# Optimization experiments

Measured on AMD Instinct MI355X. Metric: run time of the kernel, lower is better.

## Reference

```python
import jax, jax.numpy as jnp
import numpy as np

NUM_USERS = 50000
NUM_ITEMS = 50000
N_NODES = NUM_USERS + NUM_ITEMS
NNZ = 3200000
EMB_DIM = 64
N_LAYERS = 3
BATCH = 16384


def setup_inputs() -> dict:
    key = jax.random.key(0)
    ks = jax.random.split(key, 7)
    user_emb = 0.1 * jax.random.normal(ks[0], (NUM_USERS, EMB_DIM), dtype=jnp.float32)
    item_emb = 0.1 * jax.random.normal(ks[1], (NUM_ITEMS, EMB_DIM), dtype=jnp.float32)
    edge_val = jax.random.uniform(ks[2], (NNZ,), dtype=jnp.float32)
    edge_src = jax.random.randint(ks[3], (NNZ,), 0, N_NODES, dtype=jnp.int32)
    edge_dst = jax.random.randint(ks[4], (NNZ,), 0, N_NODES, dtype=jnp.int32)
    users = jax.random.randint(ks[5], (BATCH,), 0, NUM_USERS, dtype=jnp.int32)
    items = jax.random.randint(ks[6], (BATCH,), 0, NUM_ITEMS, dtype=jnp.int32)
    return {"user_emb": user_emb, "item_emb": item_emb, "edge_val": edge_val,
            "edge_src": edge_src, "edge_dst": edge_dst, "users": users, "items": items}


def _computer(user_emb, item_emb, edge_val, edge_src, edge_dst):
    # LightGCN propagation: all_emb <- A @ all_emb, mean over layer outputs (incl. layer 0)
    all_emb = jnp.concatenate([user_emb, item_emb], axis=0)  # [N, D]
    acc = all_emb
    for _ in range(N_LAYERS):
        msg = edge_val[:, None] * all_emb[edge_src]          # [nnz, D]
        all_emb = jax.ops.segment_sum(msg, edge_dst, num_segments=N_NODES)
        acc = acc + all_emb
    light_out = acc / jnp.float32(N_LAYERS + 1)
    return light_out[:NUM_USERS], light_out[NUM_USERS:]


def reference(user_emb, item_emb, edge_val, edge_src, edge_dst, users, items):
    all_users, all_items = _computer(user_emb, item_emb, edge_val, edge_src, edge_dst)
    users_emb = all_users[users]                              # [B, D]
    items_emb = all_items[items]                              # [B, D]
    gamma = jnp.sum(users_emb * items_emb, axis=1)            # [B]
    return gamma
```

## Files before the change

kernel.cpp:

```cpp
#include <hip/hip_runtime.h>

#define NUM_USERS 50000
#define NUM_ITEMS 50000
#define N_NODES   100000
#define NNZ       3200000
#define EMB_DIM   64
#define N_LAYERS  3
#define BATCH     16384

#define NBUCK 512
#define ABITS 8
#define NODES_PER_BUCK 256
#define TILE_EDGES 8192
#define NBUCK_USED ((N_NODES + NODES_PER_BUCK - 1) / NODES_PER_BUCK)
#define CAP 9216

typedef unsigned long long ull;
typedef float v2f __attribute__((ext_vector_type(2)));

__device__ inline unsigned bf16pair(float a, float b) {
    unsigned ua = __float_as_uint(a), ub = __float_as_uint(b);
    unsigned r0 = (ua + 0x7fffu + ((ua >> 16) & 1u)) >> 16;
    unsigned r1 = (ub + 0x7fffu + ((ub >> 16) & 1u)) >> 16;
    return r0 | (r1 << 16);
}
__device__ inline float blo(unsigned u) { return __uint_as_float(u << 16); }
__device__ inline float bhi(unsigned u) { return __uint_as_float(u & 0xffff0000u); }

__device__ inline void pkfma(v2f& d, v2f a, v2f b) {
    asm("v_pk_fma_f32 %0, %1, %2, %0" : "+v"(d) : "v"(a), "v"(b));
}

__device__ inline void accP(v2f& sA, v2f& sB, v2f& sC, v2f& sD, uint4 g, unsigned r) {
    float w = (float)(r >> 17);
    v2f w2 = {w, w};
    v2f e0 = {blo(g.x), bhi(g.x)};
    v2f e1 = {blo(g.y), bhi(g.y)};
    v2f e2 = {blo(g.z), bhi(g.z)};
    v2f e3 = {blo(g.w), bhi(g.w)};
    pkfma(sA, e0, w2);
    pkfma(sB, e1, w2);
    pkfma(sC, e2, w2);
    pkfma(sD, e3, w2);
}

__device__ inline uint4 gath(const unsigned char* __restrict__ base, unsigned r, unsigned dOff) {
    unsigned off = ((r & 0x1FFFFu) << 7) + dOff;
    return *(const uint4*)(base + off);
}

__global__ void init_emb_kernel(const float* __restrict__ ue,
                                const float* __restrict__ ie,
                                unsigned* __restrict__ E0,
                                int* __restrict__ bucketCursor,
                                unsigned char* __restrict__ flags,
                                const int* __restrict__ users,
                                const int* __restrict__ items) {
    int idx = blockIdx.x * blockDim.x + threadIdx.x;
    if (blockIdx.x == 0 && threadIdx.x < 256) {
        bucketCursor[threadIdx.x]       = threadIdx.x * CAP;
        bucketCursor[threadIdx.x + 256] = (threadIdx.x + 256) * CAP;
    }
    if (idx < BATCH) {
        flags[users[idx]] = 1;
    } else if (idx < 2 * BATCH) {
        flags[NUM_USERS + items[idx - BATCH]] = 1;
    }
    const int total = N_NODES * (EMB_DIM / 4);
    if (idx >= total) return;
    const int uoff = NUM_USERS * (EMB_DIM / 4);
    float4 v;
    if (idx < uoff) v = ((const float4*)ue)[idx];
    else            v = ((const float4*)ie)[idx - uoff];
    uint2 h;
    h.x = bf16pair(v.x, v.y);
    h.y = bf16pair(v.z, v.w);
    ((uint2*)E0)[idx] = h;
}

__global__ void partA_kernel(const float* __restrict__ ev,
                             const int*  __restrict__ es,
                             const int*  __restrict__ ed,
                             int* __restrict__ bucketCursor,
                             ull* __restrict__ tmp) {
    __shared__ int hist[NBUCK];
    __shared__ int base[NBUCK];
    __shared__ int cnt2[NBUCK];
    int tid = threadIdx.x;
    int e0 = blockIdx.x * TILE_EDGES;

    int      mySrc[8], myDst[8];
    unsigned myQ[8];

    for (int i = tid; i < NBUCK; i += 1024) hist[i] = 0;
    __syncthreads();

    #pragma unroll
    for (int k = 0; k < 8; ++k) {
        int e = e0 + k * 1024 + tid;
        if (e < NNZ) {
            mySrc[k] = es[e];
            myDst[k] = ed[e];
            myQ[k]   = (unsigned)fminf(ev[e] * 32768.f + 0.5f, 32767.f);
            atomicAdd(&hist[((unsigned)myDst[k]) >> ABITS], 1);
        } else {
            myDst[k] = -1;
        }
    }
    __syncthreads();

    for (int i = tid; i < NBUCK; i += 1024) {
        int c = hist[i];
        base[i] = c ? atomicAdd(&bucketCursor[i], c) : 0;
        cnt2[i] = 0;
    }
    __syncthreads();

    #pragma unroll
    for (int k = 0; k < 8; ++k) {
        int dst = myDst[k];
        if (dst < 0) continue;
        int b = ((unsigned)dst) >> ABITS;
        int pos = base[b] + atomicAdd(&cnt2[b], 1);
        if (pos < (b + 1) * CAP) {
            ull rec = (ull)(unsigned)(mySrc[k] | ((dst & (NODES_PER_BUCK - 1)) << 17))
                    | ((ull)myQ[k] << 25);
            tmp[pos] = rec;
        }
    }
}

__global__ void partB_kernel(const ull* __restrict__ tmp,
                             const int* __restrict__ bucketCursor,
                             int* __restrict__ rowStart,
                             int* __restrict__ deg,
                             unsigned* __restrict__ sorted) {
    __shared__ int cnt[NODES_PER_BUCK];
    __shared__ int sc[NODES_PER_BUCK];
    __shared__ int cur[NODES_PER_BUCK];
    int b = blockIdx.x;
    int tid = threadIdx.x;
    int nodeLo = b << ABITS;
    int startE = b * CAP;
    int endE   = bucketCursor[b];

    if (tid < NODES_PER_BUCK) cnt[tid] = 0;
    __syncthreads();

    ull myRec[9];
    int nRec = 0;
    #pragma unroll
    for (int k = 0; k < 9; ++k) {
        int i = startE + k * 1024 + tid;
        if (i < endE) {
            myRec[k] = tmp[i];
            nRec = k + 1;
            atomicAdd(&cnt[(int)((myRec[k] >> 17) & (NODES_PER_BUCK - 1))], 1);
        }
    }
    __syncthreads();

    if (tid < NODES_PER_BUCK) sc[tid] = (cnt[tid] + 3) & ~3;
    __syncthreads();
    for (int o = 1; o < NODES_PER_BUCK; o <<= 1) {
        int add = 0;
        if (tid < NODES_PER_BUCK && tid >= o) add = sc[tid - o];
        __syncthreads();
        if (tid < NODES_PER_BUCK) sc[tid] += add;
        __syncthreads();
    }
    if (tid < NODES_PER_BUCK) {
        int node = nodeLo + tid;
        int pc = (cnt[tid] + 3) & ~3;
        int rs = startE + sc[tid] - pc;
        cur[tid] = rs;
        if (node < N_NODES) {
            rowStart[node] = rs;
            deg[node] = cnt[tid];
        }
    }
    __syncthreads();

    for (int k = 0; k < nRec; ++k) {
        ull rec = myRec[k];
        int dl = (int)((rec >> 17) & (NODES_PER_BUCK - 1));
        unsigned o = (unsigned)(rec & 0x1FFFFULL) | ((unsigned)((rec >> 25) & 0x7FFF) << 17);
        int pos = atomicAdd(&cur[dl], 1);
        if (pos < startE + CAP) sorted[pos] = o;
    }
}

__global__ void pull_kernel(const unsigned char* __restrict__ A16,
                            uint4* __restrict__ B16,
                            const unsigned* __restrict__ sorted,
                            const int* __restrict__ rowStart,
                            const int* __restrict__ deg,
                            const unsigned char* __restrict__ flags,
                            int gate) {
    int node = __builtin_amdgcn_readfirstlane((blockIdx.x << 2) + (threadIdx.x >> 6));
    if (node >= N_NODES) return;
    if (gate && flags[node] != 1) return;
    int lane = threadIdx.x & 63;
    int eg = lane >> 3;
    unsigned dOff = (unsigned)(lane & 7) << 4;
    int start = rowStart[node];
    int cnt   = deg[node];
    const unsigned* ep = sorted + start;

    v2f sA = {0.f, 0.f}, sB = {0.f, 0.f}, sC = {0.f, 0.f}, sD = {0.f, 0.f};
    int j = 0;
    while (j + 32 <= cnt) {
        uint4 R = *(const uint4*)(ep + j + (eg << 2));
        uint4 g0 = gath(A16, R.x, dOff);
        uint4 g1 = gath(A16, R.y, dOff);
        uint4 g2 = gath(A16, R.z, dOff);
        uint4 g3 = gath(A16, R.w, dOff);
        accP(sA, sB, sC, sD, g0, R.x);
        accP(sA, sB, sC, sD, g1, R.y);
        accP(sA, sB, sC, sD, g2, R.z);
        accP(sA, sB, sC, sD, g3, R.w);
        j += 32;
    }
    int rem = cnt - j;
    if (rem >= 16) {
        uint2 R = *(const uint2*)(ep + j + (eg << 1));
        uint4 g0 = gath(A16, R.x, dOff);
        uint4 g1 = gath(A16, R.y, dOff);
        accP(sA, sB, sC, sD, g0, R.x);
        accP(sA, sB, sC, sD, g1, R.y);
        j += 16; rem -= 16;
    }
    if (rem > 0) {
        int i0 = j + eg, i1 = j + 8 + eg;
        unsigned r0 = (i0 < cnt) ? ep[i0] : 0u;
        unsigned r1 = (i1 < cnt) ? ep[i1] : 0u;
        uint4 g0 = gath(A16, r0, dOff);
        uint4 g1 = gath(A16, r1, dOff);
        accP(sA, sB, sC, sD, g0, r0);
        accP(sA, sB, sC, sD, g1, r1);
    }

    sA.x += __shfl_xor(sA.x, 8, 64);  sA.y += __shfl_xor(sA.y, 8, 64);
    sB.x += __shfl_xor(sB.x, 8, 64);  sB.y += __shfl_xor(sB.y, 8, 64);
    sC.x += __shfl_xor(sC.x, 8, 64);  sC.y += __shfl_xor(sC.y, 8, 64);
    sD.x += __shfl_xor(sD.x, 8, 64);  sD.y += __shfl_xor(sD.y, 8, 64);
    sA.x += __shfl_xor(sA.x, 16, 64); sA.y += __shfl_xor(sA.y, 16, 64);
    sB.x += __shfl_xor(sB.x, 16, 64); sB.y += __shfl_xor(sB.y, 16, 64);
    sC.x += __shfl_xor(sC.x, 16, 64); sC.y += __shfl_xor(sC.y, 16, 64);
    sD.x += __shfl_xor(sD.x, 16, 64); sD.y += __shfl_xor(sD.y, 16, 64);
    sA.x += __shfl_xor(sA.x, 32, 64); sA.y += __shfl_xor(sA.y, 32, 64);
    sB.x += __shfl_xor(sB.x, 32, 64); sB.y += __shfl_xor(sB.y, 32, 64);
    sC.x += __shfl_xor(sC.x, 32, 64); sC.y += __shfl_xor(sC.y, 32, 64);
    sD.x += __shfl_xor(sD.x, 32, 64); sD.y += __shfl_xor(sD.y, 32, 64);

    if (eg == 0) {
        const float k15 = 1.f / 32768.f;
        uint4 h;
        h.x = bf16pair(sA.x * k15, sA.y * k15);
        h.y = bf16pair(sB.x * k15, sB.y * k15);
        h.z = bf16pair(sC.x * k15, sC.y * k15);
        h.w = bf16pair(sD.x * k15, sD.y * k15);
        B16[(((long long)node) << 3) + (lane & 7)] = h;
    }
}

__global__ void dot_kernel(const unsigned* __restrict__ E0,
                           const unsigned* __restrict__ B1,
                           const unsigned* __restrict__ B2,
                           const unsigned* __restrict__ B3,
                           const int* __restrict__ users,
                           const int* __restrict__ items,
                           float* __restrict__ out) {
    int t = blockIdx.x * blockDim.x + threadIdx.x;
    int b = t >> 5;
    int lane = t & 31;
    if (b >= BATCH) return;
    long long uo = ((long long)users[b] << 5) + lane;
    long long io = ((long long)(items[b] + NUM_USERS) << 5) + lane;
    unsigned a0 = E0[uo], a1 = B1[uo], a2 = B2[uo], a3 = B3[uo];
    unsigned c0 = E0[io], c1 = B1[io], c2 = B2[io], c3 = B3[io];
    float ux = (blo(a0) + blo(a1)) + (blo(a2) + blo(a3));
    float uy = (bhi(a0) + bhi(a1)) + (bhi(a2) + bhi(a3));
    float ix = (blo(c0) + blo(c1)) + (blo(c2) + blo(c3));
    float iy = (bhi(c0) + bhi(c1)) + (bhi(c2) + bhi(c3));
    float p = ux * ix + uy * iy;
    #pragma unroll
    for (int off = 16; off >= 1; off >>= 1)
        p += __shfl_xor(p, off, 64);
    if (lane == 0) out[b] = p * 0.0625f;
}

extern "C" void kernel_launch(void* const* d_in, const int* in_sizes, int n_in,
                              void* d_out, int out_size, void* d_ws, size_t ws_size,
                              hipStream_t stream) {
    const float* user_emb = (const float*)d_in[0];
    const float* item_emb = (const float*)d_in[1];
    const float* edge_val = (const float*)d_in[2];
    const int*   edge_src = (const int*)d_in[3];
    const int*   edge_dst = (const int*)d_in[4];
    const int*   users    = (const int*)d_in[5];
    const int*   items    = (const int*)d_in[6];
    float* out = (float*)d_out;

    const size_t emb16Bytes = (size_t)N_NODES * EMB_DIM * 2;
    const size_t sortBytes  = (size_t)NBUCK_USED * CAP * sizeof(unsigned);
    const size_t tmpBytes   = (size_t)NBUCK_USED * CAP * sizeof(ull);
    const size_t nodeBytes  = (size_t)N_NODES * sizeof(int);

    char* w = (char*)d_ws;
    unsigned* E0           = (unsigned*)(w); w += emb16Bytes;
    unsigned* B1           = (unsigned*)(w); w += emb16Bytes;
    unsigned* B2           = (unsigned*)(w); w += emb16Bytes;
    unsigned* B3           = (unsigned*)(w); w += emb16Bytes;
    unsigned* sorted       = (unsigned*)(w); w += sortBytes;
    ull*      tmp          = (ull*)(w);      w += tmpBytes;
    int*      deg          = (int*)(w);      w += nodeBytes;
    int*      rowStart     = (int*)(w);      w += nodeBytes;
    int*      bucketCursor = (int*)(w);      w += NBUCK * sizeof(int);
    unsigned char* flags   = (unsigned char*)(w); w += N_NODES;

    const int vecTotal   = N_NODES * (EMB_DIM / 4);
    const int initBlocks = (vecTotal + 255) / 256;
    const int tileBlocks = (NNZ + TILE_EDGES - 1) / TILE_EDGES;

    init_emb_kernel<<<initBlocks, 256, 0, stream>>>(user_emb, item_emb, E0,
                                                    bucketCursor, flags, users, items);

    partA_kernel<<<tileBlocks, 1024, 0, stream>>>(edge_val, edge_src, edge_dst,
                                                  bucketCursor, tmp);
    partB_kernel<<<NBUCK_USED, 1024, 0, stream>>>(tmp, bucketCursor,
                                                  rowStart, deg, sorted);

    const int pullBlocks = (N_NODES * 64 + 255) / 256;
    pull_kernel<<<pullBlocks, 256, 0, stream>>>((const unsigned char*)E0, (uint4*)B1,
                                                sorted, rowStart, deg, flags, 0);
    pull_kernel<<<pullBlocks, 256, 0, stream>>>((const unsigned char*)B1, (uint4*)B2,
                                                sorted, rowStart, deg, flags, 0);
    pull_kernel<<<pullBlocks, 256, 0, stream>>>((const unsigned char*)B2, (uint4*)B3,
                                                sorted, rowStart, deg, flags, 1);

    const int dotBlocks = (BATCH * 32 + 255) / 256;
    dot_kernel<<<dotBlocks, 256, 0, stream>>>(E0, B1, B2, B3, users, items, out);
}
```

Measured before the change: 277.7 us.

## Process two nodes per wave in pull kernel with software-interleaved gathers

Each wavefront in the pull kernel now handles two destination nodes instead of one. Edge records for the first 64 edges of both nodes are loaded up front with predicated tail masking, and the gathers are interleaved so more memory requests are in flight before accumulation. The reductions use packed adds, launch bounds are set, and the grid is halved. This adds register pressure and a slow generic path for nodes with more than 64 edges, and the gated layer may now do work for an unflagged node that shares a wave with a flagged one.

```diff
diff --git a/kernel.cpp b/kernel.cpp
--- a/kernel.cpp
+++ b/kernel.cpp
@@ -29,6 +29,9 @@
 
 __device__ inline void pkfma(v2f& d, v2f a, v2f b) {
     asm("v_pk_fma_f32 %0, %1, %2, %0" : "+v"(d) : "v"(a), "v"(b));
+}
+__device__ inline void pkadd(v2f& d, v2f a) {
+    asm("v_pk_add_f32 %0, %1, %0" : "+v"(d) : "v"(a));
 }
 
 __device__ inline void accP(v2f& sA, v2f& sB, v2f& sC, v2f& sD, uint4 g, unsigned r) {
@@ -47,6 +50,23 @@
 __device__ inline uint4 gath(const unsigned char* __restrict__ base, unsigned r, unsigned dOff) {
     unsigned off = ((r & 0x1FFFFu) << 7) + dOff;
     return *(const uint4*)(base + off);
+}
+
+__device__ inline uint4 predload4(const unsigned* __restrict__ ep, int j, int b4, int cnt) {
+    int i = j + b4;
+    uint4 R = *(const uint4*)(ep + i);
+    if (i + 1 > cnt) R.x = 0u;
+    if (i + 2 > cnt) R.y = 0u;
+    if (i + 3 > cnt) R.z = 0u;
+    if (i + 4 > cnt) R.w = 0u;
+    return R;
+}
+
+__device__ inline void wred(v2f& s) {
+    v2f t;
+    t.x = __shfl_xor(s.x, 8, 64);  t.y = __shfl_xor(s.y, 8, 64);  pkadd(s, t);
+    t.x = __shfl_xor(s.x, 16, 64); t.y = __shfl_xor(s.y, 16, 64); pkadd(s, t);
+    t.x = __shfl_xor(s.x, 32, 64); t.y = __shfl_xor(s.y, 32, 64); pkadd(s, t);
 }
 
 __global__ void init_emb_kernel(const float* __restrict__ ue,
@@ -190,77 +210,133 @@
     }
 }
 
-__global__ void pull_kernel(const unsigned char* __restrict__ A16,
-                            uint4* __restrict__ B16,
-                            const unsigned* __restrict__ sorted,
-                            const int* __restrict__ rowStart,
-                            const int* __restrict__ deg,
-                            const unsigned char* __restrict__ flags,
-                            int gate) {
-    int node = __builtin_amdgcn_readfirstlane((blockIdx.x << 2) + (threadIdx.x >> 6));
-    if (node >= N_NODES) return;
-    if (gate && flags[node] != 1) return;
+__global__ void __launch_bounds__(256, 4)
+pull_kernel(const unsigned char* __restrict__ A16,
+            uint4* __restrict__ B16,
+            const unsigned* __restrict__ sorted,
+            const int* __restrict__ rowStart,
+            const int* __restrict__ deg,
+            const unsigned char* __restrict__ flags,
+            int gate) {
+    int wid = __builtin_amdgcn_readfirstlane((blockIdx.x << 2) + (threadIdx.x >> 6));
+    int n0 = wid << 1;
+    if (n0 >= N_NODES) return;
     int lane = threadIdx.x & 63;
     int eg = lane >> 3;
+    int b4 = eg << 2;
     unsigned dOff = (unsigned)(lane & 7) << 4;
-    int start = rowStart[node];
-    int cnt   = deg[node];
-    const unsigned* ep = sorted + start;
-
-    v2f sA = {0.f, 0.f}, sB = {0.f, 0.f}, sC = {0.f, 0.f}, sD = {0.f, 0.f};
-    int j = 0;
-    while (j + 32 <= cnt) {
-        uint4 R = *(const uint4*)(ep + j + (eg << 2));
-        uint4 g0 = gath(A16, R.x, dOff);
-        uint4 g1 = gath(A16, R.y, dOff);
-        uint4 g2 = gath(A16, R.z, dOff);
-        uint4 g3 = gath(A16, R.w, dOff);
-        accP(sA, sB, sC, sD, g0, R.x);
-        accP(sA, sB, sC, sD, g1, R.y);
-        accP(sA, sB, sC, sD, g2, R.z);
-        accP(sA, sB, sC, sD, g3, R.w);
-        j += 32;
-    }
-    int rem = cnt - j;
-    if (rem >= 16) {
-        uint2 R = *(const uint2*)(ep + j + (eg << 1));
-        uint4 g0 = gath(A16, R.x, dOff);
-        uint4 g1 = gath(A16, R.y, dOff);
-        accP(sA, sB, sC, sD, g0, R.x);
-        accP(sA, sB, sC, sD, g1, R.y);
-        j += 16; rem -= 16;
-    }
-    if (rem > 0) {
-        int i0 = j + eg, i1 = j + 8 + eg;
-        unsigned r0 = (i0 < cnt) ? ep[i0] : 0u;
-        unsigned r1 = (i1 < cnt) ? ep[i1] : 0u;
-        uint4 g0 = gath(A16, r0, dOff);
-        uint4 g1 = gath(A16, r1, dOff);
-        accP(sA, sB, sC, sD, g0, r0);
-        accP(sA, sB, sC, sD, g1, r1);
-    }
-
-    sA.x += __shfl_xor(sA.x, 8, 64);  sA.y += __shfl_xor(sA.y, 8, 64);
-    sB.x += __shfl_xor(sB.x, 8, 64);  sB.y += __shfl_xor(sB.y, 8, 64);
-    sC.x += __shfl_xor(sC.x, 8, 64);  sC.y += __shfl_xor(sC.y, 8, 64);
-    sD.x += __shfl_xor(sD.x, 8, 64);  sD.y += __shfl_xor(sD.y, 8, 64);
-    sA.x += __shfl_xor(sA.x, 16, 64); sA.y += __shfl_xor(sA.y, 16, 64);
-    sB.x += __shfl_xor(sB.x, 16, 64); sB.y += __shfl_xor(sB.y, 16, 64);
-    sC.x += __shfl_xor(sC.x, 16, 64); sC.y += __shfl_xor(sC.y, 16, 64);
-    sD.x += __shfl_xor(sD.x, 16, 64); sD.y += __shfl_xor(sD.y, 16, 64);
-    sA.x += __shfl_xor(sA.x, 32, 64); sA.y += __shfl_xor(sA.y, 32, 64);
-    sB.x += __shfl_xor(sB.x, 32, 64); sB.y += __shfl_xor(sB.y, 32, 64);
-    sC.x += __shfl_xor(sC.x, 32, 64); sC.y += __shfl_xor(sC.y, 32, 64);
-    sD.x += __shfl_xor(sD.x, 32, 64); sD.y += __shfl_xor(sD.y, 32, 64);
+
+    bool a0 = true, a1 = true;
+    if (gate) {
+        a0 = flags[n0] == 1;
+        a1 = flags[n0 + 1] == 1;
+        if (!(a0 || a1)) return;
+    }
+    int c0 = a0 ? deg[n0] : 0;
+    int c1 = a1 ? deg[n0 + 1] : 0;
+    const unsigned* ep0 = sorted + rowStart[n0];
+    const unsigned* ep1 = sorted + rowStart[n0 + 1];
+
+    bool u0a = c0 > 0,  u0b = c0 > 32;
+    bool u1a = c1 > 0,  u1b = c1 > 32;
+
+    uint4 R0a, R1a, R0b, R1b;
+    if (u0a) R0a = predload4(ep0, 0,  b4, c0);
+    if (u1a) R1a = predload4(ep1, 0,  b4, c1);
+    if (u0b) R0b = predload4(ep0, 32, b4, c0);
+    if (u1b) R1b = predload4(ep1, 32, b4, c1);
+
+    v2f s0A = {0.f,0.f}, s0B = {0.f,0.f}, s0C = {0.f,0.f}, s0D = {0.f,0.f};
+    v2f s1A = {0.f,0.f}, s1B = {0.f,0.f}, s1C = {0.f,0.f}, s1D = {0.f,0.f};
+
+    uint4 G0a0, G0a1, G0a2, G0a3;
+    uint4 G1a0, G1a1, G1a2, G1a3;
+    uint4 G0b0, G0b1, G0b2, G0b3;
+    uint4 G1b0, G1b1, G1b2, G1b3;
+    if (u0a) {
+        G0a0 = gath(A16, R0a.x, dOff); G0a1 = gath(A16, R0a.y, dOff);
+        G0a2 = gath(A16, R0a.z, dOff); G0a3 = gath(A16, R0a.w, dOff);
+    }
+    if (u1a) {
+        G1a0 = gath(A16, R1a.x, dOff); G1a1 = gath(A16, R1a.y, dOff);
+        G1a2 = gath(A16, R1a.z, dOff); G1a3 = gath(A16, R1a.w, dOff);
+    }
+    if (u0b) {
+        G0b0 = gath(A16, R0b.x, dOff); G0b1 = gath(A16, R0b.y, dOff);
+        G0b2 = gath(A16, R0b.z, dOff); G0b3 = gath(A16, R0b.w, dOff);
+    }
+
+    if (u0a) {
+        accP(s0A, s0B, s0C, s0D, G0a0, R0a.x);
+        accP(s0A, s0B, s0C, s0D, G0a1, R0a.y);
+        accP(s0A, s0B, s0C, s0D, G0a2, R0a.z);
+        accP(s0A, s0B, s0C, s0D, G0a3, R0a.w);
+    }
+    if (u1b) {
+        G1b0 = gath(A16, R1b.x, dOff); G1b1 = gath(A16, R1b.y, dOff);
+        G1b2 = gath(A16, R1b.z, dOff); G1b3 = gath(A16, R1b.w, dOff);
+    }
+    if (u0b) {
+        accP(s0A, s0B, s0C, s0D, G0b0, R0b.x);
+        accP(s0A, s0B, s0C, s0D, G0b1, R0b.y);
+        accP(s0A, s0B, s0C, s0D, G0b2, R0b.z);
+        accP(s0A, s0B, s0C, s0D, G0b3, R0b.w);
+    }
+    if (u1a) {
+        accP(s1A, s1B, s1C, s1D, G1a0, R1a.x);
+        accP(s1A, s1B, s1C, s1D, G1a1, R1a.y);
+        accP(s1A, s1B, s1C, s1D, G1a2, R1a.z);
+        accP(s1A, s1B, s1C, s1D, G1a3, R1a.w);
+    }
+    if (u1b) {
+        accP(s1A, s1B, s1C, s1D, G1b0, R1b.x);
+        accP(s1A, s1B, s1C, s1D, G1b1, R1b.y);
+        accP(s1A, s1B, s1C, s1D, G1b2, R1b.z);
+        accP(s1A, s1B, s1C, s1D, G1b3, R1b.w);
+    }
+
+    if (__builtin_expect((c0 > 64) || (c1 > 64), 0)) {
+        for (int j = 64; j < c0; j += 16) {
+            int i0 = j + eg, i1 = j + 8 + eg;
+            unsigned r0 = (i0 < c0) ? ep0[i0] : 0u;
+            unsigned r1 = (i1 < c0) ? ep0[i1] : 0u;
+            uint4 g0 = gath(A16, r0, dOff);
+            uint4 g1 = gath(A16, r1, dOff);
+            accP(s0A, s0B, s0C, s0D, g0, r0);
+            accP(s0A, s0B, s0C, s0D, g1, r1);
+        }
+        for (int j = 64; j < c1; j += 16) {
+            int i0 = j + eg, i1 = j + 8 + eg;
+            unsigned r0 = (i0 < c1) ? ep1[i0] : 0u;
+            unsigned r1 = (i1 < c1) ? ep1[i1] : 0u;
+            uint4 g0 = gath(A16, r0, dOff);
+            uint4 g1 = gath(A16, r1, dOff);
+            accP(s1A, s1B, s1C, s1D, g0, r0);
+            accP(s1A, s1B, s1C, s1D, g1, r1);
+        }
+    }
+
+    wred(s0A); wred(s1A); wred(s0B); wred(s1B);
+    wred(s0C); wred(s1C); wred(s0D); wred(s1D);
 
     if (eg == 0) {
         const float k15 = 1.f / 32768.f;
-        uint4 h;
-        h.x = bf16pair(sA.x * k15, sA.y * k15);
-        h.y = bf16pair(sB.x * k15, sB.y * k15);
-        h.z = bf16pair(sC.x * k15, sC.y * k15);
-        h.w = bf16pair(sD.x * k15, sD.y * k15);
-        B16[(((long long)node) << 3) + (lane & 7)] = h;
+        if (a0) {
+            uint4 h;
+            h.x = bf16pair(s0A.x * k15, s0A.y * k15);
+            h.y = bf16pair(s0B.x * k15, s0B.y * k15);
+            h.z = bf16pair(s0C.x * k15, s0C.y * k15);
+            h.w = bf16pair(s0D.x * k15, s0D.y * k15);
+            B16[(((long long)n0) << 3) + (lane & 7)] = h;
+        }
+        if (a1) {
+            uint4 h;
+            h.x = bf16pair(s1A.x * k15, s1A.y * k15);
+            h.y = bf16pair(s1B.x * k15, s1B.y * k15);
+            h.z = bf16pair(s1C.x * k15, s1C.y * k15);
+            h.w = bf16pair(s1D.x * k15, s1D.y * k15);
+            B16[(((long long)(n0 + 1)) << 3) + (lane & 7)] = h;
+        }
     }
 }
 
@@ -331,7 +407,7 @@
     partB_kernel<<<NBUCK_USED, 1024, 0, stream>>>(tmp, bucketCursor,
                                                   rowStart, deg, sorted);
 
-    const int pullBlocks = (N_NODES * 64 + 255) / 256;
+    const int pullBlocks = ((N_NODES / 2) * 64 + 255) / 256;
     pull_kernel<<<pullBlocks, 256, 0, stream>>>((const unsigned char*)E0, (uint4*)B1,
                                                 sorted, rowStart, deg, flags, 0);
     pull_kernel<<<pullBlocks, 256, 0, stream>>>((const unsigned char*)B1, (uint4*)B2,
```

Result: no change. 279.7 us (+0.7%).

## Sub-sort edges by source range and pull two nodes per 8-lane group without reductions

Applied to the files above, without the earlier changes.

partB now sorts each node's edges by a coarse source-range cell and zero-pads rows to multiples of four, so deg holds padded counts. The pull kernels are restructured so each 8-lane group handles two nodes, walking their edge lists directly with a fixed unrolled prefix of 48 edges. This removes the cross-lane shuffle reduction and the flags array. The gated last layer now indexes the users/items list directly instead of checking flags per node, so duplicate batch nodes are recomputed. This trades per-wave parallelism over a node's edges for more independent gathers per lane and better source locality, at the risk of load imbalance on high-degree nodes.

```diff
diff --git a/kernel.cpp b/kernel.cpp
--- a/kernel.cpp
+++ b/kernel.cpp
@@ -13,7 +13,8 @@
 #define NODES_PER_BUCK 256
 #define TILE_EDGES 8192
 #define NBUCK_USED ((N_NODES + NODES_PER_BUCK - 1) / NODES_PER_BUCK)
-#define CAP 9216
+#define CAP 9472
+#define NCELL 1024
 
 typedef unsigned long long ull;
 typedef float v2f __attribute__((ext_vector_type(2)));
@@ -49,22 +50,67 @@
     return *(const uint4*)(base + off);
 }
 
+__device__ inline void roundU(const unsigned char* __restrict__ A16,
+                              const unsigned* __restrict__ p, unsigned dOff,
+                              v2f& sA, v2f& sB, v2f& sC, v2f& sD) {
+    uint4 R = *(const uint4*)p;
+    uint4 g0 = gath(A16, R.x, dOff);
+    uint4 g1 = gath(A16, R.y, dOff);
+    uint4 g2 = gath(A16, R.z, dOff);
+    uint4 g3 = gath(A16, R.w, dOff);
+    accP(sA, sB, sC, sD, g0, R.x);
+    accP(sA, sB, sC, sD, g1, R.y);
+    accP(sA, sB, sC, sD, g2, R.z);
+    accP(sA, sB, sC, sD, g3, R.w);
+}
+
+__device__ inline void pull_pair(const unsigned char* __restrict__ A16,
+                                 uint4* __restrict__ B16,
+                                 const unsigned* __restrict__ sorted,
+                                 const int* __restrict__ rowStart,
+                                 const int* __restrict__ deg,
+                                 int nA, int nB, int d8, unsigned dOff) {
+    int dA = deg[nA], dB = deg[nB];
+    const unsigned* pA = sorted + rowStart[nA];
+    const unsigned* pB = sorted + rowStart[nB];
+
+    v2f s00 = {0.f,0.f}, s01 = {0.f,0.f}, s02 = {0.f,0.f}, s03 = {0.f,0.f};
+    v2f s10 = {0.f,0.f}, s11 = {0.f,0.f}, s12 = {0.f,0.f}, s13 = {0.f,0.f};
+
+    #pragma unroll
+    for (int base = 0; base < 48; base += 4) {
+        if (dA > base) roundU(A16, pA + base, dOff, s00, s01, s02, s03);
+        if (dB > base) roundU(A16, pB + base, dOff, s10, s11, s12, s13);
+    }
+    if (__builtin_expect((dA > 48) || (dB > 48), 0)) {
+        for (int base = 48; base < dA; base += 4)
+            roundU(A16, pA + base, dOff, s00, s01, s02, s03);
+        for (int base = 48; base < dB; base += 4)
+            roundU(A16, pB + base, dOff, s10, s11, s12, s13);
+    }
+
+    const float k15 = 1.f / 32768.f;
+    uint4 h;
+    h.x = bf16pair(s00.x * k15, s00.y * k15);
+    h.y = bf16pair(s01.x * k15, s01.y * k15);
+    h.z = bf16pair(s02.x * k15, s02.y * k15);
+    h.w = bf16pair(s03.x * k15, s03.y * k15);
+    B16[(((long long)nA) << 3) + d8] = h;
+    h.x = bf16pair(s10.x * k15, s10.y * k15);
+    h.y = bf16pair(s11.x * k15, s11.y * k15);
+    h.z = bf16pair(s12.x * k15, s12.y * k15);
+    h.w = bf16pair(s13.x * k15, s13.y * k15);
+    B16[(((long long)nB) << 3) + d8] = h;
+}
+
 __global__ void init_emb_kernel(const float* __restrict__ ue,
                                 const float* __restrict__ ie,
                                 unsigned* __restrict__ E0,
-                                int* __restrict__ bucketCursor,
-                                unsigned char* __restrict__ flags,
-                                const int* __restrict__ users,
-                                const int* __restrict__ items) {
+                                int* __restrict__ bucketCursor) {
     int idx = blockIdx.x * blockDim.x + threadIdx.x;
     if (blockIdx.x == 0 && threadIdx.x < 256) {
         bucketCursor[threadIdx.x]       = threadIdx.x * CAP;
         bucketCursor[threadIdx.x + 256] = (threadIdx.x + 256) * CAP;
-    }
-    if (idx < BATCH) {
-        flags[users[idx]] = 1;
-    } else if (idx < 2 * BATCH) {
-        flags[NUM_USERS + items[idx - BATCH]] = 1;
     }
     const int total = N_NODES * (EMB_DIM / 4);
     if (idx >= total) return;
@@ -135,19 +181,21 @@
                              int* __restrict__ rowStart,
                              int* __restrict__ deg,
                              unsigned* __restrict__ sorted) {
-    __shared__ int cnt[NODES_PER_BUCK];
-    __shared__ int sc[NODES_PER_BUCK];
-    __shared__ int cur[NODES_PER_BUCK];
+    __shared__ int cnt[NCELL];
+    __shared__ int nsc[NODES_PER_BUCK];
+    __shared__ int nstart[NODES_PER_BUCK];
+    __shared__ int cur[NCELL];
     int b = blockIdx.x;
     int tid = threadIdx.x;
     int nodeLo = b << ABITS;
     int startE = b * CAP;
     int endE   = bucketCursor[b];
 
-    if (tid < NODES_PER_BUCK) cnt[tid] = 0;
+    cnt[tid] = 0;
     __syncthreads();
 
     ull myRec[9];
+    int myCell[9];
     int nRec = 0;
     #pragma unroll
     for (int k = 0; k < 9; ++k) {
@@ -155,113 +203,100 @@
         if (i < endE) {
             myRec[k] = tmp[i];
             nRec = k + 1;
-            atomicAdd(&cnt[(int)((myRec[k] >> 17) & (NODES_PER_BUCK - 1))], 1);
+            unsigned src = (unsigned)(myRec[k] & 0x1FFFFULL);
+            int q = (int)(src >> 15); if (q > 3) q = 3;
+            int dl = (int)((myRec[k] >> 17) & (NODES_PER_BUCK - 1));
+            myCell[k] = (dl << 2) + q;
+            atomicAdd(&cnt[myCell[k]], 1);
         }
     }
     __syncthreads();
 
-    if (tid < NODES_PER_BUCK) sc[tid] = (cnt[tid] + 3) & ~3;
+    int p4 = 0;
+    if (tid < NODES_PER_BUCK) {
+        int tot = cnt[tid*4] + cnt[tid*4+1] + cnt[tid*4+2] + cnt[tid*4+3];
+        p4 = (tot + 3) & ~3;
+        nsc[tid] = p4;
+    }
     __syncthreads();
     for (int o = 1; o < NODES_PER_BUCK; o <<= 1) {
         int add = 0;
-        if (tid < NODES_PER_BUCK && tid >= o) add = sc[tid - o];
+        if (tid < NODES_PER_BUCK && tid >= o) add = nsc[tid - o];
         __syncthreads();
-        if (tid < NODES_PER_BUCK) sc[tid] += add;
+        if (tid < NODES_PER_BUCK) nsc[tid] += add;
         __syncthreads();
     }
     if (tid < NODES_PER_BUCK) {
+        int ns = startE + nsc[tid] - p4;
+        nstart[tid] = ns;
         int node = nodeLo + tid;
-        int pc = (cnt[tid] + 3) & ~3;
-        int rs = startE + sc[tid] - pc;
-        cur[tid] = rs;
         if (node < N_NODES) {
-            rowStart[node] = rs;
-            deg[node] = cnt[tid];
+            rowStart[node] = ns;
+            deg[node] = p4;
         }
+    }
+    __syncthreads();
+
+    {
+        int n = tid >> 2, q = tid & 3;
+        int c = nstart[n];
+        if (q > 0) c += cnt[n*4];
+        if (q > 1) c += cnt[n*4+1];
+        if (q > 2) c += cnt[n*4+2];
+        cur[tid] = c;
     }
     __syncthreads();
 
     for (int k = 0; k < nRec; ++k) {
         ull rec = myRec[k];
-        int dl = (int)((rec >> 17) & (NODES_PER_BUCK - 1));
         unsigned o = (unsigned)(rec & 0x1FFFFULL) | ((unsigned)((rec >> 25) & 0x7FFF) << 17);
-        int pos = atomicAdd(&cur[dl], 1);
+        int pos = atomicAdd(&cur[myCell[k]], 1);
         if (pos < startE + CAP) sorted[pos] = o;
     }
-}
-
-__global__ void pull_kernel(const unsigned char* __restrict__ A16,
-                            uint4* __restrict__ B16,
-                            const unsigned* __restrict__ sorted,
-                            const int* __restrict__ rowStart,
-                            const int* __restrict__ deg,
-                            const unsigned char* __restrict__ flags,
-                            int gate) {
-    int node = __builtin_amdgcn_readfirstlane((blockIdx.x << 2) + (threadIdx.x >> 6));
-    if (node >= N_NODES) return;
-    if (gate && flags[node] != 1) return;
+    __syncthreads();
+
+    if (tid < NODES_PER_BUCK) {
+        int tot = cnt[tid*4] + cnt[tid*4+1] + cnt[tid*4+2] + cnt[tid*4+3];
+        int end = nstart[tid] + ((tot + 3) & ~3);
+        for (int p = nstart[tid] + tot; p < end; ++p)
+            if (p < startE + CAP) sorted[p] = 0;
+    }
+}
+
+__global__ void __launch_bounds__(256, 6)
+pull_sync_kernel(const unsigned char* __restrict__ A16,
+                 uint4* __restrict__ B16,
+                 const unsigned* __restrict__ sorted,
+                 const int* __restrict__ rowStart,
+                 const int* __restrict__ deg) {
+    int wid = (blockIdx.x << 2) + (threadIdx.x >> 6);
+    if (wid >= N_NODES / 16) return;
     int lane = threadIdx.x & 63;
     int eg = lane >> 3;
-    unsigned dOff = (unsigned)(lane & 7) << 4;
-    int start = rowStart[node];
-    int cnt   = deg[node];
-    const unsigned* ep = sorted + start;
-
-    v2f sA = {0.f, 0.f}, sB = {0.f, 0.f}, sC = {0.f, 0.f}, sD = {0.f, 0.f};
-    int j = 0;
-    while (j + 32 <= cnt) {
-        uint4 R = *(const uint4*)(ep + j + (eg << 2));
-        uint4 g0 = gath(A16, R.x, dOff);
-        uint4 g1 = gath(A16, R.y, dOff);
-        uint4 g2 = gath(A16, R.z, dOff);
-        uint4 g3 = gath(A16, R.w, dOff);
-        accP(sA, sB, sC, sD, g0, R.x);
-        accP(sA, sB, sC, sD, g1, R.y);
-        accP(sA, sB, sC, sD, g2, R.z);
-        accP(sA, sB, sC, sD, g3, R.w);
-        j += 32;
-    }
-    int rem = cnt - j;
-    if (rem >= 16) {
-        uint2 R = *(const uint2*)(ep + j + (eg << 1));
-        uint4 g0 = gath(A16, R.x, dOff);
-        uint4 g1 = gath(A16, R.y, dOff);
-        accP(sA, sB, sC, sD, g0, R.x);
-        accP(sA, sB, sC, sD, g1, R.y);
-        j += 16; rem -= 16;
-    }
-    if (rem > 0) {
-        int i0 = j + eg, i1 = j + 8 + eg;
-        unsigned r0 = (i0 < cnt) ? ep[i0] : 0u;
-        unsigned r1 = (i1 < cnt) ? ep[i1] : 0u;
-        uint4 g0 = gath(A16, r0, dOff);
-        uint4 g1 = gath(A16, r1, dOff);
-        accP(sA, sB, sC, sD, g0, r0);
-        accP(sA, sB, sC, sD, g1, r1);
-    }
-
-    sA.x += __shfl_xor(sA.x, 8, 64);  sA.y += __shfl_xor(sA.y, 8, 64);
-    sB.x += __shfl_xor(sB.x, 8, 64);  sB.y += __shfl_xor(sB.y, 8, 64);
-    sC.x += __shfl_xor(sC.x, 8, 64);  sC.y += __shfl_xor(sC.y, 8, 64);
-    sD.x += __shfl_xor(sD.x, 8, 64);  sD.y += __shfl_xor(sD.y, 8, 64);
-    sA.x += __shfl_xor(sA.x, 16, 64); sA.y += __shfl_xor(sA.y, 16, 64);
-    sB.x += __shfl_xor(sB.x, 16, 64); sB.y += __shfl_xor(sB.y, 16, 64);
-    sC.x += __shfl_xor(sC.x, 16, 64); sC.y += __shfl_xor(sC.y, 16, 64);
-    sD.x += __shfl_xor(sD.x, 16, 64); sD.y += __shfl_xor(sD.y, 16, 64);
-    sA.x += __shfl_xor(sA.x, 32, 64); sA.y += __shfl_xor(sA.y, 32, 64);
-    sB.x += __shfl_xor(sB.x, 32, 64); sB.y += __shfl_xor(sB.y, 32, 64);
-    sC.x += __shfl_xor(sC.x, 32, 64); sC.y += __shfl_xor(sC.y, 32, 64);
-    sD.x += __shfl_xor(sD.x, 32, 64); sD.y += __shfl_xor(sD.y, 32, 64);
-
-    if (eg == 0) {
-        const float k15 = 1.f / 32768.f;
-        uint4 h;
-        h.x = bf16pair(sA.x * k15, sA.y * k15);
-        h.y = bf16pair(sB.x * k15, sB.y * k15);
-        h.z = bf16pair(sC.x * k15, sC.y * k15);
-        h.w = bf16pair(sD.x * k15, sD.y * k15);
-        B16[(((long long)node) << 3) + (lane & 7)] = h;
-    }
+    int d8 = lane & 7;
+    unsigned dOff = (unsigned)d8 << 4;
+    int nA = (wid << 4) + (eg << 1);
+    pull_pair(A16, B16, sorted, rowStart, deg, nA, nA + 1, d8, dOff);
+}
+
+__global__ void __launch_bounds__(256, 6)
+pull_gated_kernel(const unsigned char* __restrict__ A16,
+                  uint4* __restrict__ B16,
+                  const unsigned* __restrict__ sorted,
+                  const int* __restrict__ rowStart,
+                  const int* __restrict__ deg,
+                  const int* __restrict__ users,
+                  const int* __restrict__ items) {
+    int wid = (blockIdx.x << 2) + (threadIdx.x >> 6);
+    if (wid >= (2 * BATCH) / 16) return;
+    int lane = threadIdx.x & 63;
+    int eg = lane >> 3;
+    int d8 = lane & 7;
+    unsigned dOff = (unsigned)d8 << 4;
+    int e = (wid << 4) + (eg << 1);
+    int nA = (e     < BATCH) ? users[e]     : NUM_USERS + items[e - BATCH];
+    int nB = (e + 1 < BATCH) ? users[e + 1] : NUM_USERS + items[e + 1 - BATCH];
+    pull_pair(A16, B16, sorted, rowStart, deg, nA, nB, d8, dOff);
 }
 
 __global__ void dot_kernel(const unsigned* __restrict__ E0,
@@ -317,27 +352,27 @@
     int*      deg          = (int*)(w);      w += nodeBytes;
     int*      rowStart     = (int*)(w);      w += nodeBytes;
     int*      bucketCursor = (int*)(w);      w += NBUCK * sizeof(int);
-    unsigned char* flags   = (unsigned char*)(w); w += N_NODES;
 
     const int vecTotal   = N_NODES * (EMB_DIM / 4);
     const int initBlocks = (vecTotal + 255) / 256;
     const int tileBlocks = (NNZ + TILE_EDGES - 1) / TILE_EDGES;
 
-    init_emb_kernel<<<initBlocks, 256, 0, stream>>>(user_emb, item_emb, E0,
-                                                    bucketCursor, flags, users, items);
+    init_emb_kernel<<<initBlocks, 256, 0, stream>>>(user_emb, item_emb, E0, bucketCursor);
 
     partA_kernel<<<tileBlocks, 1024, 0, stream>>>(edge_val, edge_src, edge_dst,
                                                   bucketCursor, tmp);
     partB_kernel<<<NBUCK_USED, 1024, 0, stream>>>(tmp, bucketCursor,
                                                   rowStart, deg, sorted);
 
-    const int pullBlocks = (N_NODES * 64 + 255) / 256;
-    pull_kernel<<<pullBlocks, 256, 0, stream>>>((const unsigned char*)E0, (uint4*)B1,
-                                                sorted, rowStart, deg, flags, 0);
-    pull_kernel<<<pullBlocks, 256, 0, stream>>>((const unsigned char*)B1, (uint4*)B2,
-                                                sorted, rowStart, deg, flags, 0);
-    pull_kernel<<<pullBlocks, 256, 0, stream>>>((const unsigned char*)B2, (uint4*)B3,
-                                                sorted, rowStart, deg, flags, 1);
+    const int syncBlocks = (N_NODES / 16 + 3) / 4;
+    pull_sync_kernel<<<syncBlocks, 256, 0, stream>>>((const unsigned char*)E0, (uint4*)B1,
+                                                     sorted, rowStart, deg);
+    pull_sync_kernel<<<syncBlocks, 256, 0, stream>>>((const unsigned char*)B1, (uint4*)B2,
+                                                     sorted, rowStart, deg);
+
+    const int gatedBlocks = ((2 * BATCH) / 16 + 3) / 4;
+    pull_gated_kernel<<<gatedBlocks, 256, 0, stream>>>((const unsigned char*)B2, (uint4*)B3,
+                                                       sorted, rowStart, deg, users, items);
 
     const int dotBlocks = (BATCH * 32 + 255) / 256;
     dot_kernel<<<dotBlocks, 256, 0, stream>>>(E0, B1, B2, B3, users, items, out);
```

Result: slower. 296.0 us (+6.6%).
